# Kernel optimization log

Measured on AMD Instinct MI355X. Metric: run time of the kernel, lower is better.

## Reference

```python
import jax, jax.numpy as jnp
import numpy as np

K = 9          # neighbors (module default k=9, dilation=1 -> plain top-k)
COUT = 256     # out_channels
BN_EPS = 1e-5


def setup_inputs() -> dict:
    key = jax.random.key(0)
    k1, k2 = jax.random.split(key, 2)
    x = jax.random.normal(k1, (8, 128, 2048, 1), jnp.float32)          # [B,C,N,1]
    W = jax.random.normal(k2, (COUT, 2 * 128), jnp.float32) * 0.05     # 1x1 conv weight [Cout, 2C]
    gamma = jnp.ones((COUT,), jnp.float32)                             # BN affine scale
    beta = jnp.zeros((COUT,), jnp.float32)                             # BN affine shift
    return {"x": x, "W": W, "gamma": gamma, "beta": beta}


def reference(x, W, gamma, beta):
    # x: [B, C, N, 1] channels-first point features
    xt = jnp.transpose(x[..., 0], (0, 2, 1))                           # [B, N, C]
    B, N, C = xt.shape

    # --- dense KNN graph (matrix form): squared euclidean distance, k nearest ---
    sq = jnp.sum(xt * xt, axis=-1)                                     # [B, N]
    dist = sq[:, :, None] - 2.0 * jnp.einsum('bnc,bmc->bnm', xt, xt) + sq[:, None, :]
    _, nn_idx = jax.lax.top_k(-dist, K)                                # [B, N, K] neighbor indices

    # --- EdgeConv gather: x_i = center, x_j = neighbor ---
    x_j = jax.vmap(lambda f, i: f[i])(xt, nn_idx)                      # [B, N, K, C]
    x_i = xt[:, :, None, :]                                            # [B, N, 1, C]
    feat = jnp.concatenate(
        [jnp.broadcast_to(x_i, (B, N, K, C)), x_j - x_i], axis=-1)     # [B, N, K, 2C]

    # --- 1x1 conv (no bias) as GEMM over channel dim ---
    h = jnp.einsum('bnkc,oc->bnko', feat, W)                           # [B, N, K, Cout]

    # --- BatchNorm2d (training-mode batch stats over B,N,K per channel) ---
    mean = jnp.mean(h, axis=(0, 1, 2))
    var = jnp.var(h, axis=(0, 1, 2))
    hn = (h - mean) * jax.lax.rsqrt(var + BN_EPS) * gamma + beta

    # --- ReLU then max over k neighbors ---
    out = jnp.max(jax.nn.relu(hn), axis=2)                             # [B, N, Cout]
    return jnp.transpose(out, (0, 2, 1))                               # [B, Cout, N]
```

## Files before the change

### kernel.cpp

```cpp
#include <hip/hip_runtime.h>
#include <float.h>
#include <math.h>

#define BATCH 8
#define CHN   128
#define NPTS  2048
#define KNN   9
#define NOUT  256
#define TOTCNT (BATCH*NPTS*KNN)

typedef __attribute__((ext_vector_type(8))) short short8;
typedef __attribute__((ext_vector_type(4))) float f32x4;

__device__ __forceinline__ unsigned short f2bf(float f) {
    unsigned int u = __float_as_uint(f);
    unsigned int r = (u + 0x7FFFu + ((u >> 16) & 1u)) >> 16;
    return (unsigned short)r;
}
__device__ __forceinline__ float bf2f(unsigned short h) {
    return __uint_as_float(((unsigned int)h) << 16);
}

__global__ __launch_bounds__(256) void prep_kernel(const float* __restrict__ x,
                                                   const float* __restrict__ W,
                                                   unsigned short* __restrict__ xhi,
                                                   unsigned short* __restrict__ xlo,
                                                   unsigned short* __restrict__ whi,
                                                   unsigned short* __restrict__ wlo,
                                                   float* __restrict__ sqh,
                                                   float* __restrict__ stats) {
    __shared__ float xt[128 * 65];
    __shared__ float psq[256];
    const int b = blockIdx.x, tid = threadIdx.x;
    if (blockIdx.y == 32) {
        stats[b * 512 + tid] = 0.f;
        stats[b * 512 + 256 + tid] = 0.f;
#pragma unroll
        for (int e = 0; e < 32; ++e) {
            int idx = e * 256 + tid;
            int r = b * 64 + (idx >> 7), c = idx & 127;
            float v = (r < 256) ? (W[r * 256 + c] - W[r * 256 + 128 + c])
                                : W[(r - 256) * 256 + 128 + c];
            unsigned short h = f2bf(v);
            float hf = bf2f(h);
            whi[r * 128 + c] = h;
            wlo[r * 128 + c] = f2bf(v - hf);
        }
        return;
    }
    const int n0 = blockIdx.y * 64;
#pragma unroll 4
    for (int p = 0; p < 32; ++p) {
        int c = p * 4 + (tid >> 6), n = tid & 63;
        xt[c * 65 + n] = x[((size_t)b * CHN + c) * NPTS + n0 + n];
    }
    __syncthreads();
    const int n = tid >> 2, cq = tid & 3;
    size_t row = (size_t)(b * NPTS + n0 + n) * CHN;
    float s = 0.f;
#pragma unroll 8
    for (int j = 0; j < 32; ++j) {
        int c = cq * 32 + j;
        float f = xt[c * 65 + n];
        unsigned short h = f2bf(f);
        float hf = bf2f(h);
        unsigned short l = f2bf(f - hf);
        xhi[row + c] = h;
        xlo[row + c] = l;
        s += f * f;
    }
    psq[tid] = s;
    __syncthreads();
    if (tid < 64)
        sqh[b * NPTS + n0 + tid] =
            0.5f * (psq[tid*4] + psq[tid*4+1] + psq[tid*4+2] + psq[tid*4+3]);
}

__global__ __launch_bounds__(256) void knnpq_mfma(const unsigned short* __restrict__ xhi,
                                                  const unsigned short* __restrict__ xlo,
                                                  const float* __restrict__ sqh,
                                                  const unsigned short* __restrict__ whi,
                                                  const unsigned short* __restrict__ wlo,
                                                  float* __restrict__ pd,
                                                  int* __restrict__ pi,
                                                  float* __restrict__ p,
                                                  unsigned short* __restrict__ q) {
    __shared__ __align__(16) float dts[4 * 64 * 36];

    const int tid = threadIdx.x;
    const int b = blockIdx.x;
    const int wv = tid >> 6, lane = tid & 63;
    const int quad = lane >> 4, col = lane & 15;
    const int koff = quad * 8;
    const size_t xb = (size_t)b * NPTS * CHN;

    if (blockIdx.z >= 4) {
        const int nt = blockIdx.y >> 2;
        const int ot = ((blockIdx.y & 3) << 2) | (blockIdx.z - 4);
        const int nbase = nt * 256 + wv * 64;
        const int obase = ot * 32;

        f32x4 acc[4][2];
#pragma unroll
        for (int i = 0; i < 4; ++i)
#pragma unroll
            for (int j = 0; j < 2; ++j) acc[i][j] = (f32x4)0.f;

        for (int chk = 0; chk < 4; ++chk) {
            short8 ah[4], al[4];
#pragma unroll
            for (int i = 0; i < 4; ++i) {
                size_t g = xb + (size_t)(nbase + i * 16 + col) * CHN + chk * 32 + koff;
                ah[i] = *(const short8*)&xhi[g];
                al[i] = *(const short8*)&xlo[g];
            }
#pragma unroll
            for (int j = 0; j < 2; ++j) {
                size_t g = (size_t)(obase + j * 16 + col) * CHN + chk * 32 + koff;
                short8 bh = *(const short8*)&whi[g];
                short8 bl = *(const short8*)&wlo[g];
#pragma unroll
                for (int i = 0; i < 4; ++i) {
                    acc[i][j] = __builtin_amdgcn_mfma_f32_16x16x32_bf16(ah[i], bh, acc[i][j], 0, 0, 0);
                    acc[i][j] = __builtin_amdgcn_mfma_f32_16x16x32_bf16(ah[i], bl, acc[i][j], 0, 0, 0);
                    acc[i][j] = __builtin_amdgcn_mfma_f32_16x16x32_bf16(al[i], bh, acc[i][j], 0, 0, 0);
                }
            }
        }
#pragma unroll
        for (int i = 0; i < 4; ++i)
#pragma unroll
            for (int j = 0; j < 2; ++j) {
                int oc = (obase + j * 16 + col) & 255;
#pragma unroll
                for (int r = 0; r < 4; ++r) {
                    int n = nbase + i * 16 + quad * 4 + r;
                    size_t off = (size_t)(b * NPTS + n) * NOUT + oc;
                    if (ot < 8) p[off] = acc[i][j][r];
                    else        q[off] = f2bf(acc[i][j][r]);
                }
            }
        return;
    }

    const int q0 = blockIdx.y * 64, ms = blockIdx.z;
    const int msbase = ms * 512;
    const int mcol0 = wv * 32;
    float* dtw = &dts[wv * 64 * 36];

    float dl[KNN]; int il[KNN];
#pragma unroll
    for (int k = 0; k < KNN; ++k) { dl[k] = FLT_MAX; il[k] = 0; }

    auto ins = [&](float v, int idx) {
        if (v < dl[KNN - 1]) {
            bool c0b = v < dl[0];
#pragma unroll
            for (int k = KNN - 1; k >= 1; --k) {
                bool sh   = v < dl[k - 1];
                bool here = v < dl[k];
                float nd = sh ? dl[k - 1] : (here ? v : dl[k]);
                int   ni = sh ? il[k - 1] : (here ? idx : il[k]);
                dl[k] = nd; il[k] = ni;
            }
            if (c0b) { dl[0] = v; il[0] = idx; }
        }
    };

    for (int iter = 0; iter < 4; ++iter) {
        const int mbase = msbase + iter * 128;
        float sm[2];
#pragma unroll
        for (int j = 0; j < 2; ++j)
            sm[j] = sqh[b * NPTS + mbase + mcol0 + j * 16 + col];

        f32x4 acc[4][2];
#pragma unroll
        for (int i = 0; i < 4; ++i)
#pragma unroll
            for (int j = 0; j < 2; ++j) acc[i][j] = (f32x4)0.f;

        for (int chk = 0; chk < 4; ++chk) {
            short8 ah[4], al[4];
#pragma unroll
            for (int i = 0; i < 4; ++i) {
                size_t g = xb + (size_t)(q0 + i * 16 + col) * CHN + chk * 32 + koff;
                ah[i] = *(const short8*)&xhi[g];
                al[i] = *(const short8*)&xlo[g];
            }
#pragma unroll
            for (int j = 0; j < 2; ++j) {
                size_t g = xb + (size_t)(mbase + mcol0 + j * 16 + col) * CHN + chk * 32 + koff;
                short8 bh = *(const short8*)&xhi[g];
                short8 bl = *(const short8*)&xlo[g];
#pragma unroll
                for (int i = 0; i < 4; ++i) {
                    acc[i][j] = __builtin_amdgcn_mfma_f32_16x16x32_bf16(ah[i], bh, acc[i][j], 0, 0, 0);
                    acc[i][j] = __builtin_amdgcn_mfma_f32_16x16x32_bf16(ah[i], bl, acc[i][j], 0, 0, 0);
                    acc[i][j] = __builtin_amdgcn_mfma_f32_16x16x32_bf16(al[i], bh, acc[i][j], 0, 0, 0);
                }
            }
        }

#pragma unroll
        for (int j = 0; j < 2; ++j)
#pragma unroll
            for (int i = 0; i < 4; ++i)
#pragma unroll
                for (int r = 0; r < 4; ++r) {
                    int q_ = i * 16 + quad * 4 + r;
                    dtw[q_ * 36 + j * 16 + col] = sm[j] - acc[i][j][r];
                }
        const int ibase = mbase + mcol0;
#pragma unroll
        for (int jj = 0; jj < 8; ++jj) {
            float4 v = *(const float4*)&dtw[lane * 36 + jj * 4];
            float mn4 = fminf(fminf(v.x, v.y), fminf(v.z, v.w));
            if (mn4 < dl[KNN - 1]) {
                int ib = ibase + jj * 4;
                ins(v.x, ib); ins(v.y, ib + 1); ins(v.z, ib + 2); ins(v.w, ib + 3);
            }
        }
    }

    __syncthreads();
    float* md = dts;
    int*   mi = (int*)(dts + 2304);
#pragma unroll
    for (int k = 0; k < KNN; ++k) {
        md[lane * 36 + wv * 9 + k] = dl[k];
        mi[lane * 36 + wv * 9 + k] = il[k];
    }
    __syncthreads();
    if (tid < 64) {
        int base = tid * 36;
        int p0 = 0, p1 = 0, p2 = 0, p3 = 0;
        size_t ob = ((size_t)(b * NPTS + q0 + tid) * 4 + ms) * KNN;
        for (int k = 0; k < KNN; ++k) {
            float v0 = (p0 < KNN) ? md[base + p0]      : FLT_MAX;
            float v1 = (p1 < KNN) ? md[base + 9 + p1]  : FLT_MAX;
            float v2 = (p2 < KNN) ? md[base + 18 + p2] : FLT_MAX;
            float v3 = (p3 < KNN) ? md[base + 27 + p3] : FLT_MAX;
            float best = v0; int sel = 0;
            if (v1 < best) { best = v1; sel = 1; }
            if (v2 < best) { best = v2; sel = 2; }
            if (v3 < best) { best = v3; sel = 3; }
            int idx;
            if      (sel == 0) { idx = mi[base + p0];      p0++; }
            else if (sel == 1) { idx = mi[base + 9 + p1];  p1++; }
            else if (sel == 2) { idx = mi[base + 18 + p2]; p2++; }
            else               { idx = mi[base + 27 + p3]; p3++; }
            pd[ob + k] = best;
            pi[ob + k] = idx;
        }
    }
}

__global__ __launch_bounds__(256) void stats2_kernel(const float* __restrict__ p,
                                                     const unsigned short* __restrict__ q,
                                                     const float* __restrict__ pd,
                                                     const int* __restrict__ pi,
                                                     float* __restrict__ stats,
                                                     unsigned int* __restrict__ hmm) {
    __shared__ int idx_s[16 * KNN];
    const int b = blockIdx.x, n0 = blockIdx.y * 16;
    const int o = threadIdx.x;
    if (threadIdx.x < 16) {
        size_t g = (size_t)(b * NPTS + n0 + threadIdx.x) * 36;
        const float* d = pd + g;
        const int*   i = pi + g;
        int p0 = 0, p1 = 0, p2 = 0, p3 = 0;
#pragma unroll
        for (int k = 0; k < KNN; ++k) {
            float v0 = (p0 < KNN) ? d[p0]      : FLT_MAX;
            float v1 = (p1 < KNN) ? d[9 + p1]  : FLT_MAX;
            float v2 = (p2 < KNN) ? d[18 + p2] : FLT_MAX;
            float v3 = (p3 < KNN) ? d[27 + p3] : FLT_MAX;
            float best = v0; int sel = 0;
            if (v1 < best) { best = v1; sel = 1; }
            if (v2 < best) { best = v2; sel = 2; }
            if (v3 < best) { best = v3; sel = 3; }
            int idx;
            if      (sel == 0) { idx = i[p0];      p0++; }
            else if (sel == 1) { idx = i[9 + p1];  p1++; }
            else if (sel == 2) { idx = i[18 + p2]; p2++; }
            else               { idx = i[27 + p3]; p3++; }
            idx_s[threadIdx.x * KNN + k] = idx;
        }
    }
    __syncthreads();
    const unsigned short* qb = q + (size_t)b * NPTS * NOUT + o;
    float s = 0.f, ss = 0.f;
    for (int qq = 0; qq < 16; qq += 2) {
        size_t off0 = (size_t)(b * NPTS + n0 + qq) * NOUT + o;
        size_t off1 = off0 + NOUT;
        float pv0 = p[off0], pv1 = p[off1];
        float h0[KNN], h1[KNN];
#pragma unroll
        for (int k = 0; k < KNN; ++k)
            h0[k] = bf2f(qb[(size_t)idx_s[qq * KNN + k] * NOUT]);
#pragma unroll
        for (int k = 0; k < KNN; ++k)
            h1[k] = bf2f(qb[(size_t)idx_s[(qq + 1) * KNN + k] * NOUT]);
        float mx0 = -FLT_MAX, mn0 = FLT_MAX, mx1 = -FLT_MAX, mn1 = FLT_MAX;
#pragma unroll
        for (int k = 0; k < KNN; ++k) {
            float a = pv0 + h0[k], c = pv1 + h1[k];
            s += a + c; ss += a * a + c * c;
            mx0 = fmaxf(mx0, a); mn0 = fminf(mn0, a);
            mx1 = fmaxf(mx1, c); mn1 = fminf(mn1, c);
        }
        hmm[off0] = ((unsigned int)f2bf(mx0) << 16) | f2bf(mn0);
        hmm[off1] = ((unsigned int)f2bf(mx1) << 16) | f2bf(mn1);
    }
    atomicAdd(&stats[b * 512 + o], s);
    atomicAdd(&stats[b * 512 + NOUT + o], ss);
}

__global__ __launch_bounds__(256) void final_kernel(const unsigned int* __restrict__ hmm,
                                                    const float* __restrict__ stats,
                                                    const float* __restrict__ gamma,
                                                    const float* __restrict__ beta,
                                                    float* __restrict__ out) {
    __shared__ float tr[256 * 17];
    const int b = blockIdx.x, n0 = blockIdx.y * 16;
    const int o = threadIdx.x;
    float sum = 0.f, sumsq = 0.f;
#pragma unroll
    for (int i = 0; i < 8; ++i) {
        sum   += stats[i * 512 + o];
        sumsq += stats[i * 512 + NOUT + o];
    }
    const float inv = 1.f / (float)TOTCNT;
    float mean = sum * inv;
    float var  = sumsq * inv - mean * mean;
    float g    = gamma[o] / sqrtf(var + 1e-5f);
    float bet  = beta[o];
    const bool pos = (g >= 0.f);
    for (int qq = 0; qq < 16; ++qq) {
        size_t off = (size_t)(b * NPTS + n0 + qq) * NOUT + o;
        unsigned int w = hmm[off];
        float v = bf2f(pos ? (unsigned short)(w >> 16) : (unsigned short)(w & 0xFFFFu));
        float hn = (v - mean) * g + bet;
        tr[o * 17 + qq] = fmaxf(hn, 0.f);
    }
    __syncthreads();
    int oo = threadIdx.x >> 4, qq = threadIdx.x & 15;
    for (int pass = 0; pass < 16; ++pass) {
        int o_ = pass * 16 + oo;
        out[((size_t)b * NOUT + o_) * NPTS + n0 + qq] = tr[o_ * 17 + qq];
    }
}

extern "C" void kernel_launch(void* const* d_in, const int* in_sizes, int n_in,
                              void* d_out, int out_size, void* d_ws, size_t ws_size,
                              hipStream_t stream) {
    (void)in_sizes; (void)n_in; (void)out_size; (void)ws_size;
    const float* x     = (const float*)d_in[0];
    const float* W     = (const float*)d_in[1];
    const float* gamma = (const float*)d_in[2];
    const float* beta  = (const float*)d_in[3];
    float* out = (float*)d_out;

    char* ws = (char*)d_ws;
    float*          p     = (float*)ws;
    unsigned short* q     = (unsigned short*)(ws + (16u << 20));
    unsigned short* xhi   = (unsigned short*)(ws + (24u << 20));
    unsigned short* xlo   = (unsigned short*)(ws + (28u << 20));
    unsigned int*   hmm   = (unsigned int*)(ws + (32u << 20));
    unsigned short* whi   = (unsigned short*)(ws + (48u << 20));
    unsigned short* wlo   = (unsigned short*)(ws + (48u << 20) + 131072);
    float*          pd    = (float*)(ws + (49u << 20));
    int*            pi    = (int*)  (ws + (52u << 20));
    float*          sqh   = (float*)(ws + (55u << 20));
    float*          stats = (float*)(ws + (55u << 20) + 65536);

    prep_kernel  <<<dim3(8, 33),    256, 0, stream>>>(x, W, xhi, xlo, whi, wlo, sqh, stats);
    knnpq_mfma   <<<dim3(8, 32, 8), 256, 0, stream>>>(xhi, xlo, sqh, whi, wlo, pd, pi, p, q);
    stats2_kernel<<<dim3(8, 128),   256, 0, stream>>>(p, q, pd, pi, stats, hmm);
    final_kernel <<<dim3(8, 128),   256, 0, stream>>>(hmm, stats, gamma, beta, out);
}
```

Measured before the change: 208.2 us.

## Stage query tile in swizzled LDS and shrink distance scratch buffer

The 64-row query tile (hi and lo bf16 planes) is loaded once per block into XOR-swizzled shared memory, and the MFMA A operands are read from there instead of being re-fetched from global memory every iteration. The grid mapping is changed so the batch index comes from blockIdx.z, which reorders block scheduling for cache locality. The distance scratch is processed in 16-column halves with a 20-float stride, which cuts per-wave LDS. The cost is an extra 32KB of LDS per block and an initial barrier, and the host launch must change to match the new grid mapping, but that change is not shown.

Result: slower. 244.1 us (+17.2%).

```diff
diff --git a/kernel.cpp b/kernel.cpp
--- a/kernel.cpp
+++ b/kernel.cpp
@@ -85,18 +85,20 @@
                                                   int* __restrict__ pi,
                                                   float* __restrict__ p,
                                                   unsigned short* __restrict__ q) {
-    __shared__ __align__(16) float dts[4 * 64 * 36];
+    __shared__ __align__(16) unsigned short aS[16384];
+    __shared__ __align__(16) float dts[5120];
 
     const int tid = threadIdx.x;
-    const int b = blockIdx.x;
+    const int zr = blockIdx.x;
+    const int b  = blockIdx.z;
     const int wv = tid >> 6, lane = tid & 63;
     const int quad = lane >> 4, col = lane & 15;
     const int koff = quad * 8;
     const size_t xb = (size_t)b * NPTS * CHN;
 
-    if (blockIdx.z >= 4) {
+    if (zr >= 4) {
         const int nt = blockIdx.y >> 2;
-        const int ot = ((blockIdx.y & 3) << 2) | (blockIdx.z - 4);
+        const int ot = ((blockIdx.y & 3) << 2) | (zr - 4);
         const int nbase = nt * 256 + wv * 64;
         const int obase = ot * 32;
 
@@ -143,10 +145,22 @@
         return;
     }
 
-    const int q0 = blockIdx.y * 64, ms = blockIdx.z;
+    const int q0 = blockIdx.y * 64, ms = zr;
     const int msbase = ms * 512;
     const int mcol0 = wv * 32;
-    float* dtw = &dts[wv * 64 * 36];
+
+#pragma unroll
+    for (int t = 0; t < 8; ++t) {
+        const int plane = t >> 2;
+        const int row = (t & 3) * 16 + (tid >> 4);
+        const int off = (tid & 15) << 4;
+        const unsigned short* src = plane ? xlo : xhi;
+        short8 v = *(const short8*)&src[xb + (size_t)(q0 + row) * CHN + (off >> 1)];
+        *(short8*)((char*)aS + plane * 16384 + row * 256 + (off ^ ((row & 7) << 4))) = v;
+    }
+    __syncthreads();
+
+    float* dtw = &dts[wv * 1280];
 
     float dl[KNN]; int il[KNN];
 #pragma unroll
@@ -167,6 +181,11 @@
         }
     };
 
+    const int sw  = (col & 7) << 4;
+    const int q16 = quad << 4;
+    const int cb  = col << 8;
+    const char* ab = (const char*)aS;
+
     for (int iter = 0; iter < 4; ++iter) {
         const int mbase = msbase + iter * 128;
         float sm[2];
@@ -174,25 +193,29 @@
         for (int j = 0; j < 2; ++j)
             sm[j] = sqh[b * NPTS + mbase + mcol0 + j * 16 + col];
 
+        const size_t boff = xb + (size_t)(mbase + mcol0 + col) * CHN + koff;
+        const unsigned short* bph = xhi + boff;
+        const unsigned short* bpl = xlo + boff;
+
         f32x4 acc[4][2];
 #pragma unroll
         for (int i = 0; i < 4; ++i)
 #pragma unroll
             for (int j = 0; j < 2; ++j) acc[i][j] = (f32x4)0.f;
 
+#pragma unroll
         for (int chk = 0; chk < 4; ++chk) {
+            const int o = cb + (((chk << 6) + q16) ^ sw);
             short8 ah[4], al[4];
 #pragma unroll
             for (int i = 0; i < 4; ++i) {
-                size_t g = xb + (size_t)(q0 + i * 16 + col) * CHN + chk * 32 + koff;
-                ah[i] = *(const short8*)&xhi[g];
-                al[i] = *(const short8*)&xlo[g];
+                ah[i] = *(const short8*)(ab + i * 4096 + o);
+                al[i] = *(const short8*)(ab + 16384 + i * 4096 + o);
             }
 #pragma unroll
             for (int j = 0; j < 2; ++j) {
-                size_t g = xb + (size_t)(mbase + mcol0 + j * 16 + col) * CHN + chk * 32 + koff;
-                short8 bh = *(const short8*)&xhi[g];
-                short8 bl = *(const short8*)&xlo[g];
+                short8 bh = *(const short8*)(bph + j * 2048 + chk * 32);
+                short8 bl = *(const short8*)(bpl + j * 2048 + chk * 32);
 #pragma unroll
                 for (int i = 0; i < 4; ++i) {
                     acc[i][j] = __builtin_amdgcn_mfma_f32_16x16x32_bf16(ah[i], bh, acc[i][j], 0, 0, 0);
@@ -202,23 +225,24 @@
             }
         }
 
-#pragma unroll
-        for (int j = 0; j < 2; ++j)
+        const int ibase = mbase + mcol0;
+#pragma unroll
+        for (int j = 0; j < 2; ++j) {
 #pragma unroll
             for (int i = 0; i < 4; ++i)
 #pragma unroll
                 for (int r = 0; r < 4; ++r) {
                     int q_ = i * 16 + quad * 4 + r;
-                    dtw[q_ * 36 + j * 16 + col] = sm[j] - acc[i][j][r];
+                    dtw[q_ * 20 + col] = sm[j] - acc[i][j][r];
                 }
-        const int ibase = mbase + mcol0;
-#pragma unroll
-        for (int jj = 0; jj < 8; ++jj) {
-            float4 v = *(const float4*)&dtw[lane * 36 + jj * 4];
-            float mn4 = fminf(fminf(v.x, v.y), fminf(v.z, v.w));
-            if (mn4 < dl[KNN - 1]) {
-                int ib = ibase + jj * 4;
-                ins(v.x, ib); ins(v.y, ib + 1); ins(v.z, ib + 2); ins(v.w, ib + 3);
+#pragma unroll
+            for (int jj = 0; jj < 4; ++jj) {
+                float4 v = *(const float4*)&dtw[lane * 20 + jj * 4];
+                float mn4 = fminf(fminf(v.x, v.y), fminf(v.z, v.w));
+                if (mn4 < dl[KNN - 1]) {
+                    int ib = ibase + j * 16 + jj * 4;
+                    ins(v.x, ib); ins(v.y, ib + 1); ins(v.z, ib + 2); ins(v.w, ib + 3);
+                }
             }
         }
     }
```
